# Kernel tuning notes

Hardware: AMD Instinct MI355X
Metric: run time of the kernel (lower is better)

Reference implementation:

```python
import jax, jax.numpy as jnp
from jax import lax
import numpy as np

B, CIN, COUT, H, W = 32, 64, 64, 128, 128
KH = KW = 1
STRIDE = (1, 1)
PADDING = ((0, 0), (0, 0))


def setup_inputs() -> dict:
    key = jax.random.key(0)
    k1, k2, k3, k4 = jax.random.split(key, 4)
    x_quant = jax.random.randint(k1, (B, CIN, H, W), 0, 256, dtype=jnp.int32)  # uint8 values
    weight_int8 = jax.random.randint(k2, (COUT, CIN, KH, KW), -127, 128, dtype=jnp.int32)
    weight_scale = jax.random.uniform(k3, (COUT, 1, 1, 1), dtype=jnp.float32, minval=0.001, maxval=0.02)
    weight_zero_point = jnp.zeros((COUT, 1, 1, 1), dtype=jnp.int32)
    bias_fp32 = jax.random.normal(k4, (COUT,), dtype=jnp.float32) * 0.1
    return {
        "x_quant": x_quant,
        "input_scale": jnp.float32(0.02),
        "input_zero_point": jnp.int32(128),
        "weight_int8": weight_int8,
        "weight_scale": weight_scale,
        "weight_zero_point": weight_zero_point,
        "bias_fp32": bias_fp32,
        "output_scale": jnp.float32(0.05),
        "output_zero_point": jnp.int32(128),
    }


def reference(x_quant, input_scale, input_zero_point, weight_int8, weight_scale,
              weight_zero_point, bias_fp32, output_scale, output_zero_point):
    # dequant (zero-point subtract) in fp32
    x = x_quant.astype(jnp.float32) - input_zero_point.astype(jnp.float32)          # [B,Cin,H,W]
    w = weight_int8.astype(jnp.float32) - weight_zero_point.astype(jnp.float32)     # [O,I,kh,kw]
    conv = lax.conv_general_dilated(
        x, w, window_strides=STRIDE, padding=PADDING,
        dimension_numbers=("NCHW", "OIHW", "NCHW"))                                 # [B,O,H',W']
    # requantize: per-out-channel scale + bias, round, clamp to uint8 range
    requant_scale = (input_scale * weight_scale / output_scale).reshape(1, COUT, 1, 1)
    bias_term = (bias_fp32 / output_scale).reshape(1, COUT, 1, 1)
    final_float = conv * requant_scale + bias_term
    requant = jnp.round(final_float) + output_zero_point.astype(jnp.float32)
    out_q = jnp.clip(requant, 0.0, 255.0).astype(jnp.uint8)
    return out_q
```

## Files before the change

kernel.cpp:

```cpp
#include <hip/hip_runtime.h>

#define CIN   64
#define COUT  64
#define HW    16384
#define NPIX  (32 * HW)

__global__ void prep_kernel(const int* __restrict__ w,
                            const float* __restrict__ wscale,
                            const int* __restrict__ wzp,
                            const float* __restrict__ bias,
                            const float* __restrict__ is_p,
                            const float* __restrict__ os_p,
                            const int* __restrict__ ozp_p,
                            int* __restrict__ wp,
                            float4* __restrict__ params) {
    int o = threadIdx.x;
    if (o >= COUT) return;
    int zp = wzp[o];
    int sum = 0;
    #pragma unroll
    for (int k = 0; k < 16; ++k) {
        int c0 = w[o * CIN + 4 * k + 0] - zp;
        int c1 = w[o * CIN + 4 * k + 1] - zp;
        int c2 = w[o * CIN + 4 * k + 2] - zp;
        int c3 = w[o * CIN + 4 * k + 3] - zp;
        sum += c0 + c1 + c2 + c3;
        wp[o * 16 + k] = (c0 & 0xff) | ((c1 & 0xff) << 8) |
                         ((c2 & 0xff) << 16) | ((c3 & 0xff) << 24);
    }
    float scale = is_p[0] * wscale[o] / os_p[0];
    float bterm = bias[o] / os_p[0] + (float)ozp_p[0];
    float4 pr;
    pr.x = scale;
    pr.y = bterm;
    pr.z = __int_as_float(sum);
    pr.w = 0.0f;
    params[o] = pr;
}

__global__ __launch_bounds__(256) void conv_kernel(
    const int* __restrict__ x,
    const int* __restrict__ wp_g,
    const float4* __restrict__ params_g,
    const int* __restrict__ izp_p,
    int* __restrict__ out) {

    __shared__ int4  s_wp[COUT * 4];
    __shared__ float4 s_par[COUT];

    int tid = threadIdx.x;
    s_wp[tid] = ((const int4*)wp_g)[tid];
    if (tid < COUT) s_par[tid] = params_g[tid];
    int izp_adj = izp_p[0] - 128;
    __syncthreads();

    int t = blockIdx.x * 256 + tid;
    int b = t >> 14;
    int p = t & (HW - 1);

    const int* xb = x + b * (CIN * HW) + p;

    int px[16];
    #pragma unroll
    for (int cg = 0; cg < 16; ++cg) {
        int v0 = xb[(4 * cg + 0) * HW];
        int v1 = xb[(4 * cg + 1) * HW];
        int v2 = xb[(4 * cg + 2) * HW];
        int v3 = xb[(4 * cg + 3) * HW];
        px[cg] = (v0 | (v1 << 8) | (v2 << 16) | (v3 << 24)) ^ 0x80808080;
    }

    int* ob = out + b * (COUT * HW) + p;

    #pragma unroll 8
    for (int o = 0; o < COUT; ++o) {
        int4 w0 = s_wp[o * 4 + 0];
        int4 w1 = s_wp[o * 4 + 1];
        int4 w2 = s_wp[o * 4 + 2];
        int4 w3 = s_wp[o * 4 + 3];
        float4 pr = s_par[o];
        int wsum = __float_as_int(pr.z);
        int acc = -izp_adj * wsum;

        acc = __builtin_amdgcn_sdot4(px[0],  w0.x, acc, false);
        acc = __builtin_amdgcn_sdot4(px[1],  w0.y, acc, false);
        acc = __builtin_amdgcn_sdot4(px[2],  w0.z, acc, false);
        acc = __builtin_amdgcn_sdot4(px[3],  w0.w, acc, false);
        acc = __builtin_amdgcn_sdot4(px[4],  w1.x, acc, false);
        acc = __builtin_amdgcn_sdot4(px[5],  w1.y, acc, false);
        acc = __builtin_amdgcn_sdot4(px[6],  w1.z, acc, false);
        acc = __builtin_amdgcn_sdot4(px[7],  w1.w, acc, false);
        acc = __builtin_amdgcn_sdot4(px[8],  w2.x, acc, false);
        acc = __builtin_amdgcn_sdot4(px[9],  w2.y, acc, false);
        acc = __builtin_amdgcn_sdot4(px[10], w2.z, acc, false);
        acc = __builtin_amdgcn_sdot4(px[11], w2.w, acc, false);
        acc = __builtin_amdgcn_sdot4(px[12], w3.x, acc, false);
        acc = __builtin_amdgcn_sdot4(px[13], w3.y, acc, false);
        acc = __builtin_amdgcn_sdot4(px[14], w3.z, acc, false);
        acc = __builtin_amdgcn_sdot4(px[15], w3.w, acc, false);

        float f = fmaf((float)acc, pr.x, pr.y);
        f = rintf(f);
        f = fminf(fmaxf(f, 0.0f), 255.0f);
        __builtin_nontemporal_store((int)f, ob + o * HW);
    }
}

extern "C" void kernel_launch(void* const* d_in, const int* in_sizes, int n_in,
                              void* d_out, int out_size, void* d_ws, size_t ws_size,
                              hipStream_t stream) {
    const int*   x      = (const int*)d_in[0];
    const float* is_p   = (const float*)d_in[1];
    const int*   izp_p  = (const int*)d_in[2];
    const int*   w      = (const int*)d_in[3];
    const float* wscale = (const float*)d_in[4];
    const int*   wzp    = (const int*)d_in[5];
    const float* bias   = (const float*)d_in[6];
    const float* os_p   = (const float*)d_in[7];
    const int*   ozp_p  = (const int*)d_in[8];

    int* out = (int*)d_out;

    int*    wp     = (int*)d_ws;
    float4* params = (float4*)((char*)d_ws + 4096);

    prep_kernel<<<1, 64, 0, stream>>>(w, wscale, wzp, bias, is_p, os_p, ozp_p, wp, params);

    conv_kernel<<<2048, 256, 0, stream>>>(x, wp, params, izp_p, out);
}
```

Measured before the change: 252.5 us.

## Process four pixels per thread with 128-bit vector loads and stores

Each thread now handles four consecutive pixels, loading inputs and storing outputs as 128-bit vectors and reusing each weight load across four dot-product accumulators. The grid is cut to a quarter of the blocks. This aims to reduce per-element memory instruction count and LDS weight reads, at the cost of higher register pressure and far fewer resident waves to hide memory latency.

```diff
diff --git a/kernel.cpp b/kernel.cpp
--- a/kernel.cpp
+++ b/kernel.cpp
@@ -3,7 +3,10 @@
 #define CIN   64
 #define COUT  64
 #define HW    16384
+#define HW4   4096
 #define NPIX  (32 * HW)
+
+typedef int   v4i __attribute__((ext_vector_type(4)));
 
 __global__ void prep_kernel(const int* __restrict__ w,
                             const float* __restrict__ wscale,
@@ -45,7 +48,7 @@
     const int* __restrict__ izp_p,
     int* __restrict__ out) {
 
-    __shared__ int4  s_wp[COUT * 4];
+    __shared__ int4   s_wp[COUT * 4];
     __shared__ float4 s_par[COUT];
 
     int tid = threadIdx.x;
@@ -55,54 +58,58 @@
     __syncthreads();
 
     int t = blockIdx.x * 256 + tid;
-    int b = t >> 14;
-    int p = t & (HW - 1);
+    int b = t >> 12;
+    int q = t & (HW4 - 1);
 
-    const int* xb = x + b * (CIN * HW) + p;
+    const v4i* xb = (const v4i*)(x + b * (CIN * HW)) + q;
 
-    int px[16];
+    int px0[16], px1[16], px2[16], px3[16];
     #pragma unroll
     for (int cg = 0; cg < 16; ++cg) {
-        int v0 = xb[(4 * cg + 0) * HW];
-        int v1 = xb[(4 * cg + 1) * HW];
-        int v2 = xb[(4 * cg + 2) * HW];
-        int v3 = xb[(4 * cg + 3) * HW];
-        px[cg] = (v0 | (v1 << 8) | (v2 << 16) | (v3 << 24)) ^ 0x80808080;
+        v4i v0 = xb[(4 * cg + 0) * HW4];
+        v4i v1 = xb[(4 * cg + 1) * HW4];
+        v4i v2 = xb[(4 * cg + 2) * HW4];
+        v4i v3 = xb[(4 * cg + 3) * HW4];
+        px0[cg] = (v0.x | (v1.x << 8) | (v2.x << 16) | (v3.x << 24)) ^ 0x80808080;
+        px1[cg] = (v0.y | (v1.y << 8) | (v2.y << 16) | (v3.y << 24)) ^ 0x80808080;
+        px2[cg] = (v0.z | (v1.z << 8) | (v2.z << 16) | (v3.z << 24)) ^ 0x80808080;
+        px3[cg] = (v0.w | (v1.w << 8) | (v2.w << 16) | (v3.w << 24)) ^ 0x80808080;
     }
 
-    int* ob = out + b * (COUT * HW) + p;
+    v4i* ob = (v4i*)(out + b * (COUT * HW)) + q;
 
-    #pragma unroll 8
+    #pragma unroll 2
     for (int o = 0; o < COUT; ++o) {
-        int4 w0 = s_wp[o * 4 + 0];
-        int4 w1 = s_wp[o * 4 + 1];
-        int4 w2 = s_wp[o * 4 + 2];
-        int4 w3 = s_wp[o * 4 + 3];
+        int wv[16];
+        *(int4*)(&wv[0])  = s_wp[o * 4 + 0];
+        *(int4*)(&wv[4])  = s_wp[o * 4 + 1];
+        *(int4*)(&wv[8])  = s_wp[o * 4 + 2];
+        *(int4*)(&wv[12]) = s_wp[o * 4 + 3];
         float4 pr = s_par[o];
         int wsum = __float_as_int(pr.z);
-        int acc = -izp_adj * wsum;
+        int base = -izp_adj * wsum;
 
-        acc = __builtin_amdgcn_sdot4(px[0],  w0.x, acc, false);
-        acc = __builtin_amdgcn_sdot4(px[1],  w0.y, acc, false);
-        acc = __builtin_amdgcn_sdot4(px[2],  w0.z, acc, false);
-        acc = __builtin_amdgcn_sdot4(px[3],  w0.w, acc, false);
-        acc = __builtin_amdgcn_sdot4(px[4],  w1.x, acc, false);
-        acc = __builtin_amdgcn_sdot4(px[5],  w1.y, acc, false);
-        acc = __builtin_amdgcn_sdot4(px[6],  w1.z, acc, false);
-        acc = __builtin_amdgcn_sdot4(px[7],  w1.w, acc, false);
-        acc = __builtin_amdgcn_sdot4(px[8],  w2.x, acc, false);
-        acc = __builtin_amdgcn_sdot4(px[9],  w2.y, acc, false);
-        acc = __builtin_amdgcn_sdot4(px[10], w2.z, acc, false);
-        acc = __builtin_amdgcn_sdot4(px[11], w2.w, acc, false);
-        acc = __builtin_amdgcn_sdot4(px[12], w3.x, acc, false);
-        acc = __builtin_amdgcn_sdot4(px[13], w3.y, acc, false);
-        acc = __builtin_amdgcn_sdot4(px[14], w3.z, acc, false);
-        acc = __builtin_amdgcn_sdot4(px[15], w3.w, acc, false);
+        int a0 = base, a1 = base, a2 = base, a3 = base;
+        #pragma unroll
+        for (int cg = 0; cg < 16; ++cg) {
+            a0 = __builtin_amdgcn_sdot4(px0[cg], wv[cg], a0, false);
+            a1 = __builtin_amdgcn_sdot4(px1[cg], wv[cg], a1, false);
+            a2 = __builtin_amdgcn_sdot4(px2[cg], wv[cg], a2, false);
+            a3 = __builtin_amdgcn_sdot4(px3[cg], wv[cg], a3, false);
+        }
 
-        float f = fmaf((float)acc, pr.x, pr.y);
-        f = rintf(f);
-        f = fminf(fmaxf(f, 0.0f), 255.0f);
-        __builtin_nontemporal_store((int)f, ob + o * HW);
+        float f0 = fmaf((float)a0, pr.x, pr.y);
+        float f1 = fmaf((float)a1, pr.x, pr.y);
+        float f2 = fmaf((float)a2, pr.x, pr.y);
+        float f3 = fmaf((float)a3, pr.x, pr.y);
+        f0 = fminf(fmaxf(rintf(f0), 0.0f), 255.0f);
+        f1 = fminf(fmaxf(rintf(f1), 0.0f), 255.0f);
+        f2 = fminf(fmaxf(rintf(f2), 0.0f), 255.0f);
+        f3 = fminf(fmaxf(rintf(f3), 0.0f), 255.0f);
+
+        v4i r;
+        r.x = (int)f0; r.y = (int)f1; r.z = (int)f2; r.w = (int)f3;
+        __builtin_nontemporal_store(r, ob + o * HW4);
     }
 }
 
@@ -126,5 +133,5 @@
 
     prep_kernel<<<1, 64, 0, stream>>>(w, wscale, wzp, bias, is_p, os_p, ozp_p, wp, params);
 
-    conv_kernel<<<2048, 256, 0, stream>>>(x, wp, params, izp_p, out);
+    conv_kernel<<<512, 256, 0, stream>>>(x, wp, params, izp_p, out);
 }
```

Measured after the change: 261.5 us. +3.5%, slower.

## Stage input tile into LDS via direct global-to-LDS loads with smaller blocks

Applied to the files above, without the earlier changes.

The input pixels are now loaded with global_load_lds, 16-byte direct copies from global memory into shared memory. Each wave copies two channels of 128 pixels per instruction. Threads then read their 64 channel values from LDS instead of issuing 64 strided global loads each. Block size drops from 256 to 128 threads and the grid doubles, which aims for wider per-lane loads and more blocks in flight, at the cost of 32KB of LDS per block and lower occupancy.

```diff
diff --git a/kernel.cpp b/kernel.cpp
--- a/kernel.cpp
+++ b/kernel.cpp
@@ -3,6 +3,7 @@
 #define CIN   64
 #define COUT  64
 #define HW    16384
+#define PXB   128
 #define NPIX  (32 * HW)
 
 __global__ void prep_kernel(const int* __restrict__ w,
@@ -38,39 +39,55 @@
     params[o] = pr;
 }
 
-__global__ __launch_bounds__(256) void conv_kernel(
+__global__ __launch_bounds__(128) void conv_kernel(
     const int* __restrict__ x,
     const int* __restrict__ wp_g,
     const float4* __restrict__ params_g,
     const int* __restrict__ izp_p,
     int* __restrict__ out) {
 
-    __shared__ int4  s_wp[COUT * 4];
+    __shared__ int    s_x[CIN * PXB];
+    __shared__ int4   s_wp[COUT * 4];
     __shared__ float4 s_par[COUT];
 
-    int tid = threadIdx.x;
-    s_wp[tid] = ((const int4*)wp_g)[tid];
+    const int tid  = threadIdx.x;
+    const int wave = tid >> 6;
+    const int lane = tid & 63;
+
+    const int t0 = blockIdx.x * PXB;
+    const int b  = t0 >> 14;
+    const int p0 = t0 & (HW - 1);
+    const int* xb = x + b * (CIN * HW) + p0;
+
+    #pragma unroll
+    for (int j = 0; j < 16; ++j) {
+        const int c  = (wave * 16 + j) * 2;
+        const int cl = c + (lane >> 5);
+        const int* gp = xb + cl * HW + (lane & 31) * 4;
+        __builtin_amdgcn_global_load_lds(
+            (const __attribute__((address_space(1))) int*)gp,
+            (__attribute__((address_space(3))) int*)&s_x[c * PXB],
+            16, 0, 0);
+    }
+
+    s_wp[tid]       = ((const int4*)wp_g)[tid];
+    s_wp[tid + 128] = ((const int4*)wp_g)[tid + 128];
     if (tid < COUT) s_par[tid] = params_g[tid];
-    int izp_adj = izp_p[0] - 128;
+    const int izp_adj = izp_p[0] - 128;
+
     __syncthreads();
-
-    int t = blockIdx.x * 256 + tid;
-    int b = t >> 14;
-    int p = t & (HW - 1);
-
-    const int* xb = x + b * (CIN * HW) + p;
 
     int px[16];
     #pragma unroll
     for (int cg = 0; cg < 16; ++cg) {
-        int v0 = xb[(4 * cg + 0) * HW];
-        int v1 = xb[(4 * cg + 1) * HW];
-        int v2 = xb[(4 * cg + 2) * HW];
-        int v3 = xb[(4 * cg + 3) * HW];
+        int v0 = s_x[(4 * cg + 0) * PXB + tid];
+        int v1 = s_x[(4 * cg + 1) * PXB + tid];
+        int v2 = s_x[(4 * cg + 2) * PXB + tid];
+        int v3 = s_x[(4 * cg + 3) * PXB + tid];
         px[cg] = (v0 | (v1 << 8) | (v2 << 16) | (v3 << 24)) ^ 0x80808080;
     }
 
-    int* ob = out + b * (COUT * HW) + p;
+    int* ob = out + b * (COUT * HW) + p0 + tid;
 
     #pragma unroll 8
     for (int o = 0; o < COUT; ++o) {
@@ -126,5 +143,5 @@
 
     prep_kernel<<<1, 64, 0, stream>>>(w, wscale, wzp, bias, is_p, os_p, ozp_p, wp, params);
 
-    conv_kernel<<<2048, 256, 0, stream>>>(x, wp, params, izp_p, out);
+    conv_kernel<<<4096, 128, 0, stream>>>(x, wp, params, izp_p, out);
 }
```

After: 253.9 us. Within noise of the previous version (+0.5%).
